# Performance work log

Hardware: AMD Instinct MI355X
Metric: run time of the kernel (lower is better)

Reference implementation:

```python
import jax, jax.numpy as jnp
import numpy as np

EMBED_DIM = 1024
NUM_HEADS = 16
HEAD_DIM = EMBED_DIM // NUM_HEADS
ROPE_BASE = 10000.0
NEG_INF = -1e9


def _rope_tables(T, dim, dtype=jnp.float32):
    inv_freq = 1.0 / (ROPE_BASE ** (jnp.arange(0, dim, 2, dtype=jnp.float32) / dim))
    t = jnp.arange(T, dtype=jnp.float32)
    freqs = jnp.einsum('t,f->tf', t, inv_freq)          # [T, dim/2]
    emb = jnp.concatenate([freqs, freqs], axis=-1)       # [T, dim]
    return jnp.cos(emb).astype(dtype), jnp.sin(emb).astype(dtype)


def _rotate_half(x):
    x1, x2 = jnp.split(x, 2, axis=-1)
    return jnp.concatenate([-x2, x1], axis=-1)


def setup_inputs() -> dict:
    key = jax.random.key(0)
    kx, kqkv, kout = jax.random.split(key, 3)
    B, T = 2, 2048
    x = jax.random.normal(kx, (B, T, EMBED_DIM), dtype=jnp.float32)
    # Dense kernels (no bias), glorot-ish scale
    w_qkv = jax.random.normal(kqkv, (EMBED_DIM, 3 * EMBED_DIM), dtype=jnp.float32) * (EMBED_DIM ** -0.5)
    w_out = jax.random.normal(kout, (EMBED_DIM, EMBED_DIM), dtype=jnp.float32) * (EMBED_DIM ** -0.5)
    return {"x": x, "w_qkv": w_qkv, "w_out": w_out}


def reference(x, w_qkv, w_out):
    B, T, _ = x.shape
    qkv = x @ w_qkv                                      # [B, T, 3E]
    q, k, v = jnp.split(qkv, 3, axis=-1)

    def split_heads(t):
        return t.reshape(B, T, NUM_HEADS, HEAD_DIM).transpose(0, 2, 1, 3)  # [B,H,T,D]

    q, k, v = split_heads(q), split_heads(k), split_heads(v)

    cos, sin = _rope_tables(T, HEAD_DIM, x.dtype)        # [T, D]
    cos = cos[None, None, :, :]
    sin = sin[None, None, :, :]
    q = q * cos + _rotate_half(q) * sin
    k = k * cos + _rotate_half(k) * sin

    scale = jnp.sqrt(jnp.asarray(HEAD_DIM, dtype=jnp.float32)).astype(x.dtype)
    scores = jnp.einsum('bhqd,bhkd->bhqk', q, k) / scale  # [B,H,T,T]
    causal = jnp.tril(jnp.ones((T, T), dtype=bool))[None, None, :, :]
    scores = jnp.where(causal, scores, jnp.asarray(NEG_INF, dtype=x.dtype))
    probs = jax.nn.softmax(scores, axis=-1)
    out = jnp.einsum('bhqk,bhkd->bhqd', probs, v)         # [B,H,T,D]
    out = out.transpose(0, 2, 1, 3).reshape(B, T, EMBED_DIM)
    return out @ w_out
```

## Files before the change

kernel.cpp:

```cpp
#include <hip/hip_runtime.h>
#include <hip/hip_bf16.h>
#include <cstdint>

#define DI __device__ __forceinline__

using u16x8  = __attribute__((ext_vector_type(8))) unsigned short;
using u32x4  = __attribute__((ext_vector_type(4))) unsigned int;
using bf16x8 = __attribute__((ext_vector_type(8))) __bf16;
using f32x4  = __attribute__((ext_vector_type(4))) float;


DI unsigned short f2bf(float f) {
  unsigned u = __builtin_bit_cast(unsigned, f);
  u += 0x7fffu + ((u >> 16) & 1u);
  return (unsigned short)(u >> 16);
}
DI float bf2f(unsigned short b) {
  unsigned u = (unsigned)b << 16;
  return __builtin_bit_cast(float, u);
}
DI unsigned cvt_pk_bf16(float lo, float hi) {
  unsigned r;
  asm("v_cvt_pk_bf16_f32 %0, %1, %2" : "=v"(r) : "v"(lo), "v"(hi));
  return r;
}
DI void permlane_swap32(unsigned& a, unsigned& b) {
  asm("v_permlane32_swap_b32 %0, %1" : "+v"(a), "+v"(b));
}
DI void permlane_swap16(unsigned& a, unsigned& b) {
  asm("v_permlane16_swap_b32 %0, %1" : "+v"(a), "+v"(b));
}

DI void gld_lds16(const void* g, void* l) {
  __builtin_amdgcn_global_load_lds(
      (const __attribute__((address_space(1))) void*)(uintptr_t)g,
      (__attribute__((address_space(3))) void*)(uint32_t)(uintptr_t)l,
      16, 0, 0);
}


__global__ __launch_bounds__(256) void cvt_bf16_kernel(const float* __restrict__ in,
                                                        unsigned short* __restrict__ out, int n) {
  int i = (blockIdx.x * 256 + threadIdx.x) * 8;
  if (i >= n) return;
  float4 v0 = *(const float4*)(in + i);
  float4 v1 = *(const float4*)(in + i + 4);
  u16x8 o;
  o[0] = f2bf(v0.x); o[1] = f2bf(v0.y); o[2] = f2bf(v0.z); o[3] = f2bf(v0.w);
  o[4] = f2bf(v1.x); o[5] = f2bf(v1.y); o[6] = f2bf(v1.z); o[7] = f2bf(v1.w);
  *(u16x8*)(out + i) = o;
}

__global__ __launch_bounds__(256) void transpose_cvt_kernel(const float* __restrict__ in,
                                                             unsigned short* __restrict__ out,
                                                             int K, int N) {
  __shared__ float tile[32][33];
  int n0 = blockIdx.x * 32, k0 = blockIdx.y * 32;
  int tx = threadIdx.x & 31, ty = threadIdx.x >> 5;
#pragma unroll
  for (int i = 0; i < 4; ++i)
    tile[ty * 4 + i][tx] = in[(size_t)(k0 + ty * 4 + i) * N + n0 + tx];
  __syncthreads();
#pragma unroll
  for (int i = 0; i < 4; ++i)
    out[(size_t)(n0 + ty * 4 + i) * K + k0 + tx] = f2bf(tile[tx][ty * 4 + i]);
}


template <int MODE>
__global__ __launch_bounds__(256)
void gemm_tn(const unsigned short* __restrict__ A, const unsigned short* __restrict__ B,
             unsigned short* __restrict__ q_out, unsigned short* __restrict__ k_out,
             unsigned short* __restrict__ v_out, float* __restrict__ c_out,
             int M, int N, int K) {
  __shared__ __align__(16) char smem[2][16384];
  const int tid = threadIdx.x;
  const int lane = tid & 63, wave = tid >> 6;
  const int wm = wave >> 1, wn = wave & 1;

  constexpr int BANDW = (MODE == 0) ? 3 : 1;
  const int id = blockIdx.x;
  const int xcd = id & 7, rr = id >> 3;
  const int bx = xcd * BANDW + rr % BANDW;
  const int by = rr / BANDW;
  const int m0 = by << 7, n0 = bx << 7;

  const int r15 = lane & 15, g4 = lane >> 4;

  const size_t Ks = (size_t)K;
  const unsigned short* aptr = A + (size_t)(m0 + wave * 16 + r15) * Ks + g4 * 8;
  const unsigned short* bptr = B + (size_t)(n0 + wave * 16 + r15) * Ks + g4 * 8;

  f32x4 acc[4][4] = {};
  const int NT = K >> 5;

  auto stage = [&](int buf, int kt) {
    const unsigned short* ak = aptr + kt * 32;
    const unsigned short* bk = bptr + kt * 32;
    char* sA = &smem[buf][0] + wave * 1024;
    char* sB = &smem[buf][8192] + wave * 1024;
    gld_lds16(ak, sA);
    gld_lds16(ak + 64 * Ks, sA + 4096);
    gld_lds16(bk, sB);
    gld_lds16(bk + 64 * Ks, sB + 4096);
  };

  stage(0, 0);
  __syncthreads();
  for (int kt = 0; kt < NT; ++kt) {
    int buf = kt & 1;
    if (kt + 1 < NT) stage(buf ^ 1, kt + 1);
    const char* base = &smem[buf][0];
    bf16x8 af[4], bfr[4];
#pragma unroll
    for (int mt = 0; mt < 4; ++mt)
      af[mt] = *(const bf16x8*)(base + ((wm * 4 + mt) * 64 + lane) * 16);
#pragma unroll
    for (int nt = 0; nt < 4; ++nt)
      bfr[nt] = *(const bf16x8*)(base + 8192 + ((wn * 4 + nt) * 64 + lane) * 16);
#pragma unroll
    for (int mt = 0; mt < 4; ++mt)
#pragma unroll
      for (int nt = 0; nt < 4; ++nt)
        acc[mt][nt] = __builtin_amdgcn_mfma_f32_16x16x32_bf16(af[mt], bfr[nt], acc[mt][nt], 0, 0, 0);
    __syncthreads();
  }

  const int gm0 = m0 + wm * 64, gn0 = n0 + wn * 64;
  if constexpr (MODE == 0) {
    const int region = gn0 >> 10;
    const int h = (gn0 & 1023) >> 6;
    if (region <= 1) {
      unsigned short* dst = (region == 0) ? q_out : k_out;
      const float qs = (region == 0) ? (0.125f * 1.44269504088896341f) : 1.0f;
#pragma unroll
      for (int mt = 0; mt < 4; ++mt) {
#pragma unroll
        for (int r = 0; r < 4; ++r) {
          int mrow = gm0 + mt * 16 + g4 * 4 + r;
          int b = mrow >> 11, t = mrow & 2047;
          unsigned short* rowp = dst + (((size_t)(b * 16 + h) * 2048 + t) << 6);
          float tf = (float)t;
#pragma unroll
          for (int nt = 0; nt < 2; ++nt) {
            int j = nt * 16 + r15;
            float invf = exp2f((float)j * -0.4152410118609203f);
            float ang = tf * invf;
            float sv, cv;
            sincosf(ang, &sv, &cv);
            float x1 = acc[mt][nt][r], x2 = acc[mt][nt + 2][r];
            rowp[j]      = f2bf((x1 * cv - x2 * sv) * qs);
            rowp[j + 32] = f2bf((x2 * cv + x1 * sv) * qs);
          }
        }
      }
    } else {
      const int b = gm0 >> 11, t0 = gm0 & 2047;
      unsigned short* vhead = v_out + ((size_t)(b * 16 + h) * 64) * 2048;
      short* tb = (short*)(&smem[0][0] + wave * 8192);
#pragma unroll
      for (int p = 0; p < 2; ++p) {
#pragma unroll
        for (int np = 0; np < 2; ++np)
#pragma unroll
          for (int mt = 0; mt < 4; ++mt)
#pragma unroll
            for (int pr = 0; pr < 2; ++pr) {
              unsigned pk = cvt_pk_bf16(acc[mt][2 * p + np][2 * pr], acc[mt][2 * p + np][2 * pr + 1]);
              *(unsigned*)(tb + (np * 16 + r15) * 72 + mt * 16 + g4 * 4 + pr * 2) = pk;
            }
#pragma unroll
        for (int cc = 0; cc < 4; ++cc) {
          int dl = cc * 8 + (lane >> 3);
          int tc = (lane & 7) * 8;
          u16x8 vv = *(const u16x8*)(tb + dl * 72 + tc);
          *(u16x8*)(vhead + (size_t)(p * 32 + dl) * 2048 + t0 + tc) = vv;
        }
      }
    }
  } else {
#pragma unroll
    for (int mt = 0; mt < 4; ++mt)
#pragma unroll
      for (int r = 0; r < 4; ++r) {
        int mrow = gm0 + mt * 16 + g4 * 4 + r;
        float* rowp = c_out + (size_t)mrow * N + gn0;
#pragma unroll
        for (int nt = 0; nt < 4; ++nt)
          rowp[nt * 16 + r15] = acc[mt][nt][r];
      }
  }
}


__device__ const int RBMAP[24] = {7, 23, 20, 21, 18, 19, 17, 5,
                                  22, 6, 16, 12, 13, 14, 15, 10,
                                  0, 1, 2, 3, 8, 9, 4, 11};

__global__ __launch_bounds__(256)
void attn_fused(const unsigned short* __restrict__ qb, const unsigned short* __restrict__ kb,
                const unsigned short* __restrict__ vt, unsigned short* __restrict__ attno,
                unsigned short* __restrict__ pO, float* __restrict__ pml) {
  __shared__ __align__(16) char ksm[2][8192];
  __shared__ __align__(16) char vsm[2][8192];

  const int tid = threadIdx.x, lane = tid & 63, wave = tid >> 6;
  const int r15 = lane & 15, g4 = lane >> 4;

  const int wg = blockIdx.x;
  const int qq = wg >> 3;
  const int bh = (wg & 7) * 4 + qq / 24;
  const int rb = RBMAP[qq % 24];
  int J, c; bool multi;
  if (rb < 8) { J = rb; c = 0; multi = false; }
  else { int rr = rb - 8; J = 8 + (rr >> 1); c = rr & 1; multi = true; }
  const int ntw = 2 * J + 2;
  const int ktmid = J + 1;
  const int kt0 = (multi && c) ? ktmid : 0;
  const int ktN = multi ? (c ? ntw : ktmid) : ntw;
  const int q0 = J << 7;
  const int q0w = q0 + wave * 32;

  const size_t hb = (size_t)bh * 2048 * 64;
  const unsigned short* Qp = qb + hb;
  const unsigned short* Kp = kb + hb;
  const unsigned short* Vp = vt + hb;

  bf16x8 qf[2][2];
#pragma unroll
  for (int mq = 0; mq < 2; ++mq)
#pragma unroll
    for (int kc = 0; kc < 2; ++kc)
      qf[mq][kc] = *(const bf16x8*)(Qp + (size_t)(q0w + mq * 16 + r15) * 64 + kc * 32 + g4 * 8);

  f32x4 o[2][4] = {};
  float mr[2] = {-INFINITY, -INFINITY};
  float lr[2] = {0.f, 0.f};

  auto stage = [&](int buf, int kt) {
    const int kv0 = kt << 6;
#pragma unroll
    for (int i = 0; i < 2; ++i) {
      int f = wave * 2 + i;
      int nt = f >> 1, kc = f & 1;
      gld_lds16(Kp + (size_t)(kv0 + nt * 16 + r15) * 64 + kc * 32 + g4 * 8, &ksm[buf][f * 1024]);
      gld_lds16(Vp + (size_t)(nt * 16 + r15) * 2048 + kv0 + kc * 32 + g4 * 8, &vsm[buf][f * 1024]);
    }
  };

  auto process = [&](int buf, int kv0, bool mask) {
    bf16x8 kf[8];
#pragma unroll
    for (int i = 0; i < 8; ++i)
      kf[i] = *(const bf16x8*)(&ksm[buf][i * 1024] + lane * 16);

    f32x4 s[4][2] = {};
    __builtin_amdgcn_s_setprio(1);
#pragma unroll
    for (int nt = 0; nt < 4; ++nt)
#pragma unroll
      for (int kc = 0; kc < 2; ++kc) {
        s[nt][0] = __builtin_amdgcn_mfma_f32_16x16x32_bf16(kf[nt * 2 + kc], qf[0][kc], s[nt][0], 0, 0, 0);
        s[nt][1] = __builtin_amdgcn_mfma_f32_16x16x32_bf16(kf[nt * 2 + kc], qf[1][kc], s[nt][1], 0, 0, 0);
      }
    __builtin_amdgcn_s_setprio(0);

    if (mask) {
#pragma unroll
      for (int nt = 0; nt < 4; ++nt)
#pragma unroll
        for (int mq = 0; mq < 2; ++mq)
#pragma unroll
          for (int r = 0; r < 4; ++r)
            if (kv0 + nt * 16 + g4 * 4 + r > q0w + mq * 16 + r15) s[nt][mq][r] = -1e9f;
    }

    bf16x8 pa[2][2];
#pragma unroll
    for (int mq = 0; mq < 2; ++mq) {
      float m0 = fmaxf(fmaxf(s[0][mq][0], s[0][mq][1]), fmaxf(s[0][mq][2], s[0][mq][3]));
      float m1 = fmaxf(fmaxf(s[1][mq][0], s[1][mq][1]), fmaxf(s[1][mq][2], s[1][mq][3]));
      float m2 = fmaxf(fmaxf(s[2][mq][0], s[2][mq][1]), fmaxf(s[2][mq][2], s[2][mq][3]));
      float m3 = fmaxf(fmaxf(s[3][mq][0], s[3][mq][1]), fmaxf(s[3][mq][2], s[3][mq][3]));
      float mx = fmaxf(fmaxf(m0, m1), fmaxf(m2, m3));
      mx = fmaxf(mx, __shfl_xor(mx, 16));
      mx = fmaxf(mx, __shfl_xor(mx, 32));
      float mnew;
      if (!__all(mx <= mr[mq] + 8.f)) {
        mnew = fmaxf(mr[mq], mx);
        float fsc = exp2f(mr[mq] - mnew);
        mr[mq] = mnew;
        lr[mq] *= fsc;
#pragma unroll
        for (int r = 0; r < 4; ++r) {
          float fr = __shfl(fsc, (g4 << 2) + r);
#pragma unroll
          for (int dt = 0; dt < 4; ++dt) o[mq][dt][r] *= fr;
        }
      } else {
        mnew = mr[mq];
      }
      float t0 = 0.f, t1 = 0.f, t2 = 0.f, t3 = 0.f;
#pragma unroll
      for (int nt = 0; nt < 4; ++nt) {
        float p0 = exp2f(s[nt][mq][0] - mnew);
        float p1 = exp2f(s[nt][mq][1] - mnew);
        float p2 = exp2f(s[nt][mq][2] - mnew);
        float p3 = exp2f(s[nt][mq][3] - mnew);
        s[nt][mq][0] = p0; s[nt][mq][1] = p1; s[nt][mq][2] = p2; s[nt][mq][3] = p3;
        if (nt == 0) t0 = (p0 + p1) + (p2 + p3);
        if (nt == 1) t1 = (p0 + p1) + (p2 + p3);
        if (nt == 2) t2 = (p0 + p1) + (p2 + p3);
        if (nt == 3) t3 = (p0 + p1) + (p2 + p3);
      }
      float ps = (t0 + t1) + (t2 + t3);
      ps += __shfl_xor(ps, 16);
      ps += __shfl_xor(ps, 32);
      lr[mq] += ps;
      unsigned p32[4][2];
#pragma unroll
      for (int nt = 0; nt < 4; ++nt) {
        p32[nt][0] = cvt_pk_bf16(s[nt][mq][0], s[nt][mq][1]);
        p32[nt][1] = cvt_pk_bf16(s[nt][mq][2], s[nt][mq][3]);
      }
#pragma unroll
      for (int kc = 0; kc < 2; ++kc) {
        u32x4 w;
#pragma unroll
        for (int pi = 0; pi < 2; ++pi) {
          unsigned a = p32[2 * kc][pi], b = p32[2 * kc + 1][pi];
          permlane_swap32(a, b);
          permlane_swap16(a, b);
          w[pi] = a;
          w[2 + pi] = b;
        }
        pa[mq][kc] = __builtin_bit_cast(bf16x8, w);
      }
    }

    bf16x8 vf[8];
#pragma unroll
    for (int i = 0; i < 8; ++i)
      vf[i] = *(const bf16x8*)(&vsm[buf][i * 1024] + lane * 16);

    __builtin_amdgcn_s_setprio(1);
#pragma unroll
    for (int kc = 0; kc < 2; ++kc)
#pragma unroll
      for (int dt = 0; dt < 4; ++dt) {
        o[0][dt] = __builtin_amdgcn_mfma_f32_16x16x32_bf16(pa[0][kc], vf[dt * 2 + kc], o[0][dt], 0, 0, 0);
        o[1][dt] = __builtin_amdgcn_mfma_f32_16x16x32_bf16(pa[1][kc], vf[dt * 2 + kc], o[1][dt], 0, 0, 0);
      }
    __builtin_amdgcn_s_setprio(0);
  };

  int buf = 0;
  stage(0, kt0);
  __syncthreads();
  for (int kt = kt0; kt < ktN; ++kt) {
    if (kt + 1 < ktN) stage(buf ^ 1, kt + 1);
    const int kv0 = kt << 6;
    if (kv0 <= q0w + 31)
      process(buf, kv0, kv0 + 63 > q0w);
    __syncthreads();
    buf ^= 1;
  }

  if (!multi) {
    const int b = bh >> 4, h = bh & 15;
#pragma unroll
    for (int mq = 0; mq < 2; ++mq) {
      float inv = 1.f / lr[mq];
#pragma unroll
      for (int r = 0; r < 4; ++r) {
        float ir = __shfl(inv, (g4 << 2) + r);
        int q = q0w + mq * 16 + g4 * 4 + r;
        unsigned short* rowp = attno + (size_t)(b * 2048 + q) * 1024 + h * 64;
#pragma unroll
        for (int dt = 0; dt < 4; ++dt)
          rowp[dt * 16 + r15] = f2bf(o[mq][dt][r] * ir);
      }
    }
  } else {
    const int sidx = (bh * 8 + (J - 8)) * 2 + c;
    unsigned short* po = pO + (size_t)sidx * 8192 + wave * 32 * 64;
#pragma unroll
    for (int mq = 0; mq < 2; ++mq)
#pragma unroll
      for (int r = 0; r < 4; ++r)
#pragma unroll
        for (int dt = 0; dt < 4; ++dt)
          po[(mq * 16 + g4 * 4 + r) * 64 + dt * 16 + r15] = f2bf(o[mq][dt][r]);
    if (g4 == 0) {
      float* pm = pml + sidx * 256 + wave * 32;
#pragma unroll
      for (int mq = 0; mq < 2; ++mq) {
        pm[mq * 16 + r15] = mr[mq];
        pm[128 + mq * 16 + r15] = lr[mq];
      }
    }
  }
}

__global__ __launch_bounds__(256)
void attn_combine(const unsigned short* __restrict__ pO, const float* __restrict__ pml,
                  unsigned short* __restrict__ attno) {
  const int bx = blockIdx.x;
  const int bh = bx >> 3, Jrel = bx & 7, J = 8 + Jrel;
  const int t = threadIdx.x;
  const int row = t >> 1;
  const int dh = (t & 1) << 5;
  const int s0i = (bh * 8 + Jrel) * 2;
  const float* pm0 = pml + s0i * 256;
  const float* pm1 = pm0 + 256;
  float m0 = pm0[row], l0 = pm0[128 + row];
  float m1 = pm1[row], l1 = pm1[128 + row];
  float mg = fmaxf(m0, m1);
  float s0 = exp2f(m0 - mg), s1 = exp2f(m1 - mg);
  float inv = 1.f / (l0 * s0 + l1 * s1);
  s0 *= inv; s1 *= inv;
  const unsigned short* o0 = pO + (size_t)s0i * 8192 + row * 64 + dh;
  const unsigned short* o1 = o0 + 8192;
  const int b = bh >> 4, h = bh & 15;
  const int q = J * 128 + row;
  unsigned short* dst = attno + (size_t)(b * 2048 + q) * 1024 + h * 64 + dh;
#pragma unroll
  for (int dd = 0; dd < 32; dd += 8) {
    u16x8 a = *(const u16x8*)(o0 + dd);
    u16x8 bq = *(const u16x8*)(o1 + dd);
    u16x8 ov;
#pragma unroll
    for (int e = 0; e < 8; ++e)
      ov[e] = f2bf(bf2f(a[e]) * s0 + bf2f(bq[e]) * s1);
    *(u16x8*)(dst + dd) = ov;
  }
}


extern "C" void kernel_launch(void* const* d_in, const int* in_sizes, int n_in,
                              void* d_out, int out_size, void* d_ws, size_t ws_size,
                              hipStream_t stream) {
  const float* x     = (const float*)d_in[0];
  const float* w_qkv = (const float*)d_in[1];
  const float* w_out = (const float*)d_in[2];
  float* out = (float*)d_out;

  char* ws = (char*)d_ws;
  unsigned short* xb  = (unsigned short*)(ws);
  unsigned short* wqT = (unsigned short*)(ws + (8u << 20));
  unsigned short* woT = (unsigned short*)(ws + (14u << 20));
  unsigned short* qb  = (unsigned short*)(ws + (16u << 20));
  unsigned short* kb  = (unsigned short*)(ws + (24u << 20));
  unsigned short* vt  = (unsigned short*)(ws + (32u << 20));
  unsigned short* ao  = (unsigned short*)(ws + (40u << 20));
  unsigned short* pO  = xb;
  float*          pml = (float*)wqT;

  cvt_bf16_kernel<<<2048, 256, 0, stream>>>(x, xb, 4096 * 1024);
  transpose_cvt_kernel<<<dim3(96, 32), 256, 0, stream>>>(w_qkv, wqT, 1024, 3072);
  transpose_cvt_kernel<<<dim3(32, 32), 256, 0, stream>>>(w_out, woT, 1024, 1024);
  gemm_tn<0><<<768, 256, 0, stream>>>(xb, wqT, qb, kb, vt, nullptr, 4096, 3072, 1024);
  attn_fused<<<768, 256, 0, stream>>>(qb, kb, vt, ao, pO, pml);
  attn_combine<<<256, 256, 0, stream>>>(pO, pml, ao);
  gemm_tn<1><<<256, 256, 0, stream>>>(ao, woT, nullptr, nullptr, nullptr, out, 4096, 1024, 1024);
}
```

Baseline: 159.1 us.

## Use 256x256 tiles with 512-thread blocks for the fused QKV GEMM

Replaces the 128x128-tile QKV projection GEMM with a dedicated 256x256-tile kernel. It runs 8 waves per block, stages 64-wide K slices, uses a 128 KB double-buffered LDS, and wraps the MFMA loop in s_setprio. The larger tile roughly halves global-load traffic per FLOP and improves operand reuse. In exchange, only 192 blocks launch on a 256-CU part, so some CUs sit idle, and register pressure from 32 accumulator tiles per wave may hurt occupancy. The output projection becomes a separate, simplified 128-tile kernel.

```diff
diff --git a/kernel.cpp b/kernel.cpp
--- a/kernel.cpp
+++ b/kernel.cpp
@@ -67,22 +67,135 @@
 }
 
 
-template <int MODE>
+__global__ __launch_bounds__(512, 2)
+void gemm256_qkv(const unsigned short* __restrict__ A, const unsigned short* __restrict__ B,
+                 unsigned short* __restrict__ q_out, unsigned short* __restrict__ k_out,
+                 unsigned short* __restrict__ v_out, int M, int N, int K) {
+  __shared__ __align__(16) char smem[2][65536];
+  const int tid = threadIdx.x;
+  const int lane = tid & 63, wave = tid >> 6;
+  const int wr = wave >> 2, wc = wave & 3;
+  const int r15 = lane & 15, g4 = lane >> 4;
+
+  const int id = blockIdx.x;
+  const int g = (id & 7) * 24 + (id >> 3);
+  const int by = g / 12, bx = g % 12;
+  const int m0 = by << 8, n0 = bx << 8;
+
+  const size_t Ks = (size_t)K;
+  const unsigned short* aptr = A + (size_t)(m0 + wave * 32 + r15) * Ks + g4 * 8;
+  const unsigned short* bptr = B + (size_t)(n0 + wave * 32 + r15) * Ks + g4 * 8;
+
+  f32x4 acc[8][4] = {};
+  const int NT = K >> 6;
+
+  auto stage = [&](int buf, int kt) {
+    const unsigned short* ak = aptr + kt * 64;
+    const unsigned short* bk = bptr + kt * 64;
+    char* sA = &smem[buf][0]     + wave * 4096;
+    char* sB = &smem[buf][32768] + wave * 4096;
+    gld_lds16(ak,                sA);
+    gld_lds16(ak + 32,           sA + 1024);
+    gld_lds16(ak + 16 * Ks,      sA + 2048);
+    gld_lds16(ak + 16 * Ks + 32, sA + 3072);
+    gld_lds16(bk,                sB);
+    gld_lds16(bk + 32,           sB + 1024);
+    gld_lds16(bk + 16 * Ks,      sB + 2048);
+    gld_lds16(bk + 16 * Ks + 32, sB + 3072);
+  };
+
+  stage(0, 0);
+  __syncthreads();
+  for (int kt = 0; kt < NT; ++kt) {
+    const int buf = kt & 1;
+    if (kt + 1 < NT) stage(buf ^ 1, kt + 1);
+    const char* baseA = &smem[buf][0];
+    const char* baseB = &smem[buf][32768];
+#pragma unroll
+    for (int kc = 0; kc < 2; ++kc) {
+      bf16x8 af[8], bfr[4];
+#pragma unroll
+      for (int mt = 0; mt < 8; ++mt)
+        af[mt] = *(const bf16x8*)(baseA + (((wr * 8 + mt) * 2 + kc) << 10) + lane * 16);
+#pragma unroll
+      for (int nt = 0; nt < 4; ++nt)
+        bfr[nt] = *(const bf16x8*)(baseB + (((wc * 4 + nt) * 2 + kc) << 10) + lane * 16);
+      __builtin_amdgcn_s_setprio(1);
+#pragma unroll
+      for (int mt = 0; mt < 8; ++mt)
+#pragma unroll
+        for (int nt = 0; nt < 4; ++nt)
+          acc[mt][nt] = __builtin_amdgcn_mfma_f32_16x16x32_bf16(af[mt], bfr[nt], acc[mt][nt], 0, 0, 0);
+      __builtin_amdgcn_s_setprio(0);
+    }
+    __syncthreads();
+  }
+
+  const int gm0 = m0 + wr * 128, gn0 = n0 + wc * 64;
+  const int region = gn0 >> 10;
+  const int h = (gn0 & 1023) >> 6;
+  if (region <= 1) {
+    unsigned short* dst = (region == 0) ? q_out : k_out;
+    const float qs = (region == 0) ? (0.125f * 1.44269504088896341f) : 1.0f;
+#pragma unroll
+    for (int mt = 0; mt < 8; ++mt) {
+#pragma unroll
+      for (int r = 0; r < 4; ++r) {
+        int mrow = gm0 + mt * 16 + g4 * 4 + r;
+        int b = mrow >> 11, t = mrow & 2047;
+        unsigned short* rowp = dst + (((size_t)(b * 16 + h) * 2048 + t) << 6);
+        float tf = (float)t;
+#pragma unroll
+        for (int nt = 0; nt < 2; ++nt) {
+          int j = nt * 16 + r15;
+          float invf = exp2f((float)j * -0.4152410118609203f);
+          float ang = tf * invf;
+          float sv, cv;
+          sincosf(ang, &sv, &cv);
+          float x1 = acc[mt][nt][r], x2 = acc[mt][nt + 2][r];
+          rowp[j]      = f2bf((x1 * cv - x2 * sv) * qs);
+          rowp[j + 32] = f2bf((x2 * cv + x1 * sv) * qs);
+        }
+      }
+    }
+  } else {
+    const int b = gm0 >> 11, t0 = gm0 & 2047;
+    unsigned short* vhead = v_out + ((size_t)(b * 16 + h) * 64) * 2048;
+    short* tb = (short*)(&smem[0][0] + wave * 16384);
+#pragma unroll
+    for (int p = 0; p < 2; ++p) {
+#pragma unroll
+      for (int np = 0; np < 2; ++np)
+#pragma unroll
+        for (int mt = 0; mt < 8; ++mt)
+#pragma unroll
+          for (int pr = 0; pr < 2; ++pr) {
+            unsigned pk = cvt_pk_bf16(acc[mt][2 * p + np][2 * pr], acc[mt][2 * p + np][2 * pr + 1]);
+            *(unsigned*)(tb + (np * 16 + r15) * 136 + mt * 16 + g4 * 4 + pr * 2) = pk;
+          }
+#pragma unroll
+      for (int cc = 0; cc < 8; ++cc) {
+        int dl = (cc & 3) * 8 + (lane >> 3);
+        int tc = (lane & 7) * 8 + (cc >> 2) * 64;
+        u16x8 vv = *(const u16x8*)(tb + dl * 136 + tc);
+        *(u16x8*)(vhead + (size_t)(p * 32 + dl) * 2048 + t0 + tc) = vv;
+      }
+    }
+  }
+}
+
+
 __global__ __launch_bounds__(256)
-void gemm_tn(const unsigned short* __restrict__ A, const unsigned short* __restrict__ B,
-             unsigned short* __restrict__ q_out, unsigned short* __restrict__ k_out,
-             unsigned short* __restrict__ v_out, float* __restrict__ c_out,
-             int M, int N, int K) {
+void gemm_proj(const unsigned short* __restrict__ A, const unsigned short* __restrict__ B,
+               float* __restrict__ c_out, int M, int N, int K) {
   __shared__ __align__(16) char smem[2][16384];
   const int tid = threadIdx.x;
   const int lane = tid & 63, wave = tid >> 6;
   const int wm = wave >> 1, wn = wave & 1;
 
-  constexpr int BANDW = (MODE == 0) ? 3 : 1;
   const int id = blockIdx.x;
   const int xcd = id & 7, rr = id >> 3;
-  const int bx = xcd * BANDW + rr % BANDW;
-  const int by = rr / BANDW;
+  const int bx = xcd, by = rr;
   const int m0 = by << 7, n0 = bx << 7;
 
   const int r15 = lane & 15, g4 = lane >> 4;
@@ -127,69 +240,16 @@
   }
 
   const int gm0 = m0 + wm * 64, gn0 = n0 + wn * 64;
-  if constexpr (MODE == 0) {
-    const int region = gn0 >> 10;
-    const int h = (gn0 & 1023) >> 6;
-    if (region <= 1) {
-      unsigned short* dst = (region == 0) ? q_out : k_out;
-      const float qs = (region == 0) ? (0.125f * 1.44269504088896341f) : 1.0f;
-#pragma unroll
-      for (int mt = 0; mt < 4; ++mt) {
-#pragma unroll
-        for (int r = 0; r < 4; ++r) {
-          int mrow = gm0 + mt * 16 + g4 * 4 + r;
-          int b = mrow >> 11, t = mrow & 2047;
-          unsigned short* rowp = dst + (((size_t)(b * 16 + h) * 2048 + t) << 6);
-          float tf = (float)t;
-#pragma unroll
-          for (int nt = 0; nt < 2; ++nt) {
-            int j = nt * 16 + r15;
-            float invf = exp2f((float)j * -0.4152410118609203f);
-            float ang = tf * invf;
-            float sv, cv;
-            sincosf(ang, &sv, &cv);
-            float x1 = acc[mt][nt][r], x2 = acc[mt][nt + 2][r];
-            rowp[j]      = f2bf((x1 * cv - x2 * sv) * qs);
-            rowp[j + 32] = f2bf((x2 * cv + x1 * sv) * qs);
-          }
-        }
-      }
-    } else {
-      const int b = gm0 >> 11, t0 = gm0 & 2047;
-      unsigned short* vhead = v_out + ((size_t)(b * 16 + h) * 64) * 2048;
-      short* tb = (short*)(&smem[0][0] + wave * 8192);
-#pragma unroll
-      for (int p = 0; p < 2; ++p) {
-#pragma unroll
-        for (int np = 0; np < 2; ++np)
-#pragma unroll
-          for (int mt = 0; mt < 4; ++mt)
-#pragma unroll
-            for (int pr = 0; pr < 2; ++pr) {
-              unsigned pk = cvt_pk_bf16(acc[mt][2 * p + np][2 * pr], acc[mt][2 * p + np][2 * pr + 1]);
-              *(unsigned*)(tb + (np * 16 + r15) * 72 + mt * 16 + g4 * 4 + pr * 2) = pk;
-            }
-#pragma unroll
-        for (int cc = 0; cc < 4; ++cc) {
-          int dl = cc * 8 + (lane >> 3);
-          int tc = (lane & 7) * 8;
-          u16x8 vv = *(const u16x8*)(tb + dl * 72 + tc);
-          *(u16x8*)(vhead + (size_t)(p * 32 + dl) * 2048 + t0 + tc) = vv;
-        }
-      }
-    }
-  } else {
-#pragma unroll
-    for (int mt = 0; mt < 4; ++mt)
-#pragma unroll
-      for (int r = 0; r < 4; ++r) {
-        int mrow = gm0 + mt * 16 + g4 * 4 + r;
-        float* rowp = c_out + (size_t)mrow * N + gn0;
-#pragma unroll
-        for (int nt = 0; nt < 4; ++nt)
-          rowp[nt * 16 + r15] = acc[mt][nt][r];
-      }
-  }
+#pragma unroll
+  for (int mt = 0; mt < 4; ++mt)
+#pragma unroll
+    for (int r = 0; r < 4; ++r) {
+      int mrow = gm0 + mt * 16 + g4 * 4 + r;
+      float* rowp = c_out + (size_t)mrow * N + gn0;
+#pragma unroll
+      for (int nt = 0; nt < 4; ++nt)
+        rowp[nt * 16 + r15] = acc[mt][nt][r];
+    }
 }
 
 
@@ -459,8 +519,8 @@
   cvt_bf16_kernel<<<2048, 256, 0, stream>>>(x, xb, 4096 * 1024);
   transpose_cvt_kernel<<<dim3(96, 32), 256, 0, stream>>>(w_qkv, wqT, 1024, 3072);
   transpose_cvt_kernel<<<dim3(32, 32), 256, 0, stream>>>(w_out, woT, 1024, 1024);
-  gemm_tn<0><<<768, 256, 0, stream>>>(xb, wqT, qb, kb, vt, nullptr, 4096, 3072, 1024);
+  gemm256_qkv<<<192, 512, 0, stream>>>(xb, wqT, qb, kb, vt, 4096, 3072, 1024);
   attn_fused<<<768, 256, 0, stream>>>(qb, kb, vt, ao, pO, pml);
   attn_combine<<<256, 256, 0, stream>>>(pO, pml, ao);
-  gemm_tn<1><<<256, 256, 0, stream>>>(ao, woT, nullptr, nullptr, nullptr, out, 4096, 1024, 1024);
-}
+  gemm_proj<<<256, 256, 0, stream>>>(ao, woT, out, 4096, 1024, 1024);
+}
```

Result: slower. 622.3 us (+291.1%).
